# Performance work log

Hardware: AMD Instinct MI355X
Metric: run time of the kernel (lower is better)

Reference implementation:

```python
import jax, jax.numpy as jnp
import numpy as np

BN_EPS = 1e-5


def setup_inputs() -> dict:
    key = jax.random.key(0)
    k1, k2, k3, k4 = jax.random.split(key, 4)
    N, C, T, V = 32, 64, 300, 25
    K, O = 3, 64  # num_A adjacency branches, out_channels
    x = jax.random.normal(k1, (N, C, T, V), dtype=jnp.float32)
    A = jax.random.uniform(k2, (K, V, V), dtype=jnp.float32)
    # 1x1 conv weights per branch, He-style init as in conv_init (std = sqrt(2/O))
    W = jax.random.normal(k3, (K, O, C), dtype=jnp.float32) * np.sqrt(2.0 / O)
    b = jax.random.normal(k4, (K, O), dtype=jnp.float32) * 0.01
    gamma = jnp.ones((O,), dtype=jnp.float32)
    beta = jnp.zeros((O,), dtype=jnp.float32)
    return {"x": x, "A": A, "W": W, "b": b, "gamma": gamma, "beta": beta}


def reference(x, A, W, b, gamma, beta):
    # Per-branch graph aggregation over joints: xa[k] = x @ A[k] along V
    xa = jnp.einsum('nctv,kvw->knctw', x, A)            # [K,N,C,T,V]
    # Per-branch 1x1 conv (channel projection) + sum over branches
    y = jnp.einsum('koc,knctv->notv', W, xa)            # [N,O,T,V]
    y = y + b.sum(axis=0)[None, :, None, None]
    # BatchNorm2d in training mode: batch stats over (N,T,V), biased variance
    mean = jnp.mean(y, axis=(0, 2, 3), keepdims=True)
    var = jnp.mean((y - mean) ** 2, axis=(0, 2, 3), keepdims=True)
    y = (y - mean) * jax.lax.rsqrt(var + BN_EPS)
    y = y * gamma[None, :, None, None] + beta[None, :, None, None]
    return jax.nn.relu(y)
```

## Files before the change

kernel.cpp:

```cpp
#include <hip/hip_runtime.h>
#include <hip/hip_bf16.h>

#define NN 32
#define CC 64
#define TT 300
#define VV 25
#define KK 3
#define OO 64
#define TB 4
#define SB (TB * VV)
#define NREP 8

#define REP_OFF 0
#define WPK_OFF 1024
#define APK_OFF 7168
#define YBF_OFF 16384
#define YBF_BYTES ((size_t)NN * OO * TT * VV * 2)
#define WS_NEED_BF16 ((size_t)YBF_OFF * 4 + YBF_BYTES)

typedef __attribute__((ext_vector_type(8))) short short8;
typedef __attribute__((ext_vector_type(4))) float f32x4;

__device__ __forceinline__ unsigned short f2bf(float f) {
    unsigned u = __builtin_bit_cast(unsigned, f);
    u += 0x7FFFu + ((u >> 16) & 1u);
    return (unsigned short)(u >> 16);
}
__device__ __forceinline__ float bf2f(unsigned short b) {
    return __builtin_bit_cast(float, (unsigned)b << 16);
}
__device__ __forceinline__ unsigned pk2(float a, float b) {
    __hip_bfloat162 h = __float22bfloat162_rn(make_float2(a, b));
    unsigned r;
    __builtin_memcpy(&r, &h, sizeof(r));
    return r;
}

__global__ __launch_bounds__(512) void prep_pack(const float* __restrict__ A,
                                                 const float* __restrict__ W,
                                                 float* __restrict__ ws) {
    const int i = blockIdx.x * 512 + threadIdx.x;
    if (i < NREP * 128) ws[REP_OFF + i] = 0.0f;
    unsigned short* Wpk = reinterpret_cast<unsigned short*>(ws + WPK_OFF);
    unsigned short* Apk = reinterpret_cast<unsigned short*>(ws + APK_OFF);
    if (i < 1536) {
        int mt = i / 384, r = i - mt * 384;
        int kap = r / 64, lane = r - kap * 64;
        int li = lane & 15, g = lane >> 4;
        int o  = mt * 16 + li;
        int k  = kap >> 1, c0 = (kap & 1) * 32 + g * 8;
        const float* wp = W + ((size_t)(k * OO + o)) * CC + c0;
#pragma unroll
        for (int e = 0; e < 8; ++e) Wpk[i * 8 + e] = f2bf(wp[e]);
    } else if (i < 1920) {
        int j = i - 1536;
        int k = j / 128, r = j - k * 128;
        int nt = r / 64, lane = r - nt * 64;
        int li = lane & 15, g = lane >> 4;
        int w = nt * 16 + li;
#pragma unroll
        for (int e = 0; e < 8; ++e) {
            int v = g * 8 + e;
            float val = (v < VV && w < VV) ? A[(k * VV + v) * VV + w] : 0.0f;
            Apk[j * 8 + e] = f2bf(val);
        }
    }
}

template <int BF16Y>
__global__ __launch_bounds__(512, 6) void gcn_main(const float* __restrict__ x,
                                                   float* __restrict__ ws,
                                                   float* __restrict__ ypre) {
    __shared__ alignas(16) unsigned short xa_s[100 * 192];
    __shared__ float stats_s[128];

    const int bid  = blockIdx.x;
    const int n    = bid / (TT / TB);
    const int t0   = (bid % (TT / TB)) * TB;
    const int tid  = threadIdx.x;
    const int lane = tid & 63;
    const int wid  = tid >> 6;
    const int li   = lane & 15;
    const int g    = lane >> 4;

    if (tid < 128) stats_s[tid] = 0.0f;

    const float* xn = x + (size_t)n * (CC * TT * VV);
    short8 xf[2];
#pragma unroll
    for (int m = 0; m < 2; ++m) {
        const int row = (wid + 8 * m) * 16 + li;
        const int c = row & 63, t = row >> 6;
        const float* xr = xn + (size_t)c * (TT * VV) + (size_t)(t0 + t) * VV + g * 8;
        float e0, e1, e2, e3, e4, e5, e6, e7;
        if (g < 3) {
            e0 = xr[0]; e1 = xr[1]; e2 = xr[2]; e3 = xr[3];
            e4 = xr[4]; e5 = xr[5]; e6 = xr[6]; e7 = xr[7];
        } else {
            e0 = xr[0];
            e1 = e2 = e3 = e4 = e5 = e6 = e7 = 0.0f;
        }
        unsigned p[4] = {pk2(e0, e1), pk2(e2, e3), pk2(e4, e5), pk2(e6, e7)};
        __builtin_memcpy(&xf[m], p, 16);
    }

    short8 afrag[6];
#pragma unroll
    for (int kn = 0; kn < 6; ++kn)
        afrag[kn] = *reinterpret_cast<const short8*>(
            reinterpret_cast<const unsigned short*>(ws + APK_OFF) + ((size_t)kn * 64 + lane) * 8);

#pragma unroll
    for (int m = 0; m < 2; ++m) {
        const int mt = wid + 8 * m;
        const int r0 = mt * 16 + g * 4;
        const int tq = r0 >> 6, c0 = r0 & 63;
        const int sa = tq * 25 + li;
        const int w1 = 16 + li;
        const bool w1v = w1 < VV;
        const int sb = tq * 25 + w1;
        unsigned short* p0 = &xa_s[sa * 192 + (c0 ^ ((sa & 7) << 3))];
        unsigned short* p1 = &xa_s[(w1v ? sb : 0) * 192 + (c0 ^ (((w1v ? sb : 0) & 7) << 3))];
#pragma unroll
        for (int k = 0; k < KK; ++k) {
            f32x4 a0 = {0.f,0.f,0.f,0.f}, a1 = {0.f,0.f,0.f,0.f};
            a0 = __builtin_amdgcn_mfma_f32_16x16x32_bf16(xf[m], afrag[k * 2 + 0], a0, 0, 0, 0);
            a1 = __builtin_amdgcn_mfma_f32_16x16x32_bf16(xf[m], afrag[k * 2 + 1], a1, 0, 0, 0);
            uint2 q0 = make_uint2(pk2(a0[0], a0[1]), pk2(a0[2], a0[3]));
            *reinterpret_cast<uint2*>(p0 + k * 64) = q0;
            if (w1v) {
                uint2 q1 = make_uint2(pk2(a1[0], a1[1]), pk2(a1[2], a1[3]));
                *reinterpret_cast<uint2*>(p1 + k * 64) = q1;
            }
        }
    }
    __syncthreads();

    const int mtC   = wid >> 1;
    const int halfC = wid & 1;
    short8 wfr[6];
#pragma unroll
    for (int kap = 0; kap < 6; ++kap)
        wfr[kap] = *reinterpret_cast<const short8*>(
            reinterpret_cast<const unsigned short*>(ws + WPK_OFF) +
            ((size_t)(mtC * 6 + kap) * 64 + lane) * 8);

    unsigned short* ybf = reinterpret_cast<unsigned short*>(ws + YBF_OFF);
    const int ttv = TT * VV;
    const int oq  = mtC * 16 + g * 4;
    const int nNt = halfC ? 3 : 4;
    const int ntBase = halfC ? 4 : 0;
    float s1[4] = {0.f,0.f,0.f,0.f}, s2[4] = {0.f,0.f,0.f,0.f};
    for (int qq = 0; qq < nNt; ++qq) {
        const int nt = ntBase + qq;
        const int srow = nt * 16 + li;
        const bool sv = srow < SB;
        const int sr = sv ? srow : 0;
        const unsigned short* xb = &xa_s[sr * 192];
        const int sw = (sr & 7) << 3;
        f32x4 y = {0.f,0.f,0.f,0.f};
#pragma unroll
        for (int kap = 0; kap < 6; ++kap) {
            const short8 xaf = *reinterpret_cast<const short8*>(xb + ((kap * 32 + g * 8) ^ sw));
            y = __builtin_amdgcn_mfma_f32_16x16x32_bf16(wfr[kap], xaf, y, 0, 0, 0);
        }
        const size_t base = ((size_t)n * OO + oq) * ttv + (size_t)t0 * VV + srow;
        float vq[4];
        if (BF16Y) {
            unsigned p01 = pk2(y[0], y[1]);
            unsigned p23 = pk2(y[2], y[3]);
            if (sv) {
                ybf[base          ] = (unsigned short)p01;
                ybf[base +     ttv] = (unsigned short)(p01 >> 16);
                ybf[base + 2 * ttv] = (unsigned short)p23;
                ybf[base + 3 * ttv] = (unsigned short)(p23 >> 16);
            }
            vq[0] = bf2f((unsigned short)p01); vq[1] = bf2f((unsigned short)(p01 >> 16));
            vq[2] = bf2f((unsigned short)p23); vq[3] = bf2f((unsigned short)(p23 >> 16));
        } else {
            if (sv) {
                ypre[base          ] = y[0];
                ypre[base +     ttv] = y[1];
                ypre[base + 2 * ttv] = y[2];
                ypre[base + 3 * ttv] = y[3];
            }
            vq[0] = y[0]; vq[1] = y[1]; vq[2] = y[2]; vq[3] = y[3];
        }
#pragma unroll
        for (int j = 0; j < 4; ++j) {
            float v = sv ? vq[j] : 0.0f;
            s1[j] += v;
            s2[j] += v * v;
        }
    }
#pragma unroll
    for (int d = 1; d < 16; d <<= 1) {
#pragma unroll
        for (int j = 0; j < 4; ++j) {
            s1[j] += __shfl_xor(s1[j], d);
            s2[j] += __shfl_xor(s2[j], d);
        }
    }
    if (li == 0) {
#pragma unroll
        for (int j = 0; j < 4; ++j) {
            atomicAdd(&stats_s[oq + j], s1[j]);
            atomicAdd(&stats_s[64 + oq + j], s2[j]);
        }
    }
    __syncthreads();
    if (tid < 128)
        atomicAdd(&ws[REP_OFF + (bid & (NREP - 1)) * 128 + tid], stats_s[tid]);
}

template <int BF16Y>
__global__ __launch_bounds__(256) void bn_relu(float* __restrict__ out,
                                               const float* __restrict__ ws,
                                               const float* __restrict__ gamma,
                                               const float* __restrict__ beta) {
    const int i4 = blockIdx.x * 256 + threadIdx.x;
    const size_t i = (size_t)i4 * 4;
    const int o = (int)((i / (TT * VV)) % OO);

    float sum = 0.0f, sq = 0.0f;
#pragma unroll
    for (int r = 0; r < NREP; ++r) {
        sum += ws[REP_OFF + r * 128 + o];
        sq  += ws[REP_OFF + r * 128 + 64 + o];
    }
    const float cnt  = (float)NN * TT * VV;
    const float mean = sum / cnt;
    const float var  = sq / cnt - mean * mean;
    const float inv  = rsqrtf(var + 1e-5f);
    const float sc   = gamma[o] * inv;
    const float sh   = beta[o] - mean * sc;

    float4 v;
    if (BF16Y) {
        const ushort4 u = *reinterpret_cast<const ushort4*>(
            reinterpret_cast<const unsigned short*>(ws + YBF_OFF) + i);
        v.x = bf2f(u.x); v.y = bf2f(u.y); v.z = bf2f(u.z); v.w = bf2f(u.w);
    } else {
        v = *reinterpret_cast<float4*>(out + i);
    }
    v.x = fmaxf(v.x * sc + sh, 0.0f);
    v.y = fmaxf(v.y * sc + sh, 0.0f);
    v.z = fmaxf(v.z * sc + sh, 0.0f);
    v.w = fmaxf(v.w * sc + sh, 0.0f);
    *reinterpret_cast<float4*>(out + i) = v;
}

extern "C" void kernel_launch(void* const* d_in, const int* in_sizes, int n_in,
                              void* d_out, int out_size, void* d_ws, size_t ws_size,
                              hipStream_t stream) {
    const float* x     = (const float*)d_in[0];
    const float* A     = (const float*)d_in[1];
    const float* W     = (const float*)d_in[2];
    const float* gamma = (const float*)d_in[4];
    const float* beta  = (const float*)d_in[5];
    float* out = (float*)d_out;
    float* ws  = (float*)d_ws;

    const bool bf16y = ws_size >= WS_NEED_BF16;

    hipLaunchKernelGGL(prep_pack, dim3(4), dim3(512), 0, stream, A, W, ws);
    if (bf16y) {
        hipLaunchKernelGGL(HIP_KERNEL_NAME(gcn_main<1>), dim3(NN * (TT / TB)), dim3(512),
                           0, stream, x, ws, out);
        hipLaunchKernelGGL(HIP_KERNEL_NAME(bn_relu<1>), dim3((NN * OO * TT * VV) / 4 / 256),
                           dim3(256), 0, stream, out, ws, gamma, beta);
    } else {
        hipLaunchKernelGGL(HIP_KERNEL_NAME(gcn_main<0>), dim3(NN * (TT / TB)), dim3(512),
                           0, stream, x, ws, out);
        hipLaunchKernelGGL(HIP_KERNEL_NAME(bn_relu<0>), dim3((NN * OO * TT * VV) / 4 / 256),
                           dim3(256), 0, stream, out, ws, gamma, beta);
    }
}
```

Measured before the change: 57.40 us.

## Fuse GCN, BN stats and BN+ReLU into one cooperative persistent kernel

Adds a cooperative kernel with 480 persistent blocks that each process five (n,t) tiles. The pre-BN outputs stay in registers as packed bf16, and the batch statistics are reduced through a grid-wide sync before the normalize+ReLU is applied and written straight to the output. This removes the intermediate y round-trip through global memory and the separate bn_relu launch. In exchange it needs grid sync and enough occupancy for all 480 blocks (it falls back to the old path otherwise), the register pressure from holding five tiles of results is higher, and the output stores are scalar and strided.

```diff
diff --git a/kernel.cpp b/kernel.cpp
--- a/kernel.cpp
+++ b/kernel.cpp
@@ -1,5 +1,6 @@
 #include <hip/hip_runtime.h>
 #include <hip/hip_bf16.h>
+#include <hip/hip_cooperative_groups.h>
 
 #define NN 32
 #define CC 64
@@ -10,6 +11,9 @@
 #define TB 4
 #define SB (TB * VV)
 #define NREP 8
+#define NTILE (NN * (TT / TB))
+#define GRID 480
+#define TPB 5
 
 #define REP_OFF 0
 #define WPK_OFF 1024
@@ -67,6 +71,188 @@
     }
 }
 
+__global__ __launch_bounds__(512, 4) void gcn_coop(const float* __restrict__ x,
+                                                   float* __restrict__ ws,
+                                                   float* __restrict__ out,
+                                                   const float* __restrict__ gamma,
+                                                   const float* __restrict__ beta) {
+    __shared__ alignas(16) unsigned short xa_s[100 * 192];
+    __shared__ float stats_s[128];
+
+    const int bid  = blockIdx.x;
+    const int tid  = threadIdx.x;
+    const int lane = tid & 63;
+    const int wid  = tid >> 6;
+    const int li   = lane & 15;
+    const int g    = lane >> 4;
+    const int mtC   = wid >> 1;
+    const int halfC = wid & 1;
+    const int oq    = mtC * 16 + g * 4;
+    const int nNt   = halfC ? 3 : 4;
+    const int ntBase = halfC ? 4 : 0;
+    const int ttv = TT * VV;
+
+    if (tid < 128) stats_s[tid] = 0.0f;
+
+    short8 afrag[6], wfr[6];
+#pragma unroll
+    for (int kn = 0; kn < 6; ++kn)
+        afrag[kn] = *reinterpret_cast<const short8*>(
+            reinterpret_cast<const unsigned short*>(ws + APK_OFF) + ((size_t)kn * 64 + lane) * 8);
+#pragma unroll
+    for (int kap = 0; kap < 6; ++kap)
+        wfr[kap] = *reinterpret_cast<const short8*>(
+            reinterpret_cast<const unsigned short*>(ws + WPK_OFF) +
+            ((size_t)(mtC * 6 + kap) * 64 + lane) * 8);
+
+    unsigned yreg[TPB][4][2];
+    float s1[4] = {0.f,0.f,0.f,0.f}, s2[4] = {0.f,0.f,0.f,0.f};
+
+#pragma unroll
+    for (int ti = 0; ti < TPB; ++ti) {
+        const int tile = bid + ti * GRID;
+        const int n  = tile / (TT / TB);
+        const int t0 = (tile % (TT / TB)) * TB;
+        const float* xn = x + (size_t)n * (CC * ttv);
+
+        short8 xf[2];
+#pragma unroll
+        for (int m = 0; m < 2; ++m) {
+            const int row = (wid + 8 * m) * 16 + li;
+            const int c = row & 63, t = row >> 6;
+            const float* xr = xn + (size_t)c * ttv + (size_t)(t0 + t) * VV + g * 8;
+            float e0, e1, e2, e3, e4, e5, e6, e7;
+            if (g < 3) {
+                e0 = xr[0]; e1 = xr[1]; e2 = xr[2]; e3 = xr[3];
+                e4 = xr[4]; e5 = xr[5]; e6 = xr[6]; e7 = xr[7];
+            } else {
+                e0 = xr[0];
+                e1 = e2 = e3 = e4 = e5 = e6 = e7 = 0.0f;
+            }
+            unsigned p[4] = {pk2(e0, e1), pk2(e2, e3), pk2(e4, e5), pk2(e6, e7)};
+            __builtin_memcpy(&xf[m], p, 16);
+        }
+
+#pragma unroll
+        for (int m = 0; m < 2; ++m) {
+            const int mt = wid + 8 * m;
+            const int r0 = mt * 16 + g * 4;
+            const int tq = r0 >> 6, c0 = r0 & 63;
+            const int sa = tq * 25 + li;
+            const int w1 = 16 + li;
+            const bool w1v = w1 < VV;
+            const int sb = tq * 25 + w1;
+            unsigned short* p0 = &xa_s[sa * 192 + (c0 ^ ((sa & 7) << 3))];
+            unsigned short* p1 = &xa_s[(w1v ? sb : 0) * 192 + (c0 ^ (((w1v ? sb : 0) & 7) << 3))];
+#pragma unroll
+            for (int k = 0; k < KK; ++k) {
+                f32x4 a0 = {0.f,0.f,0.f,0.f}, a1 = {0.f,0.f,0.f,0.f};
+                a0 = __builtin_amdgcn_mfma_f32_16x16x32_bf16(xf[m], afrag[k * 2 + 0], a0, 0, 0, 0);
+                a1 = __builtin_amdgcn_mfma_f32_16x16x32_bf16(xf[m], afrag[k * 2 + 1], a1, 0, 0, 0);
+                uint2 q0 = make_uint2(pk2(a0[0], a0[1]), pk2(a0[2], a0[3]));
+                *reinterpret_cast<uint2*>(p0 + k * 64) = q0;
+                if (w1v) {
+                    uint2 q1 = make_uint2(pk2(a1[0], a1[1]), pk2(a1[2], a1[3]));
+                    *reinterpret_cast<uint2*>(p1 + k * 64) = q1;
+                }
+            }
+        }
+        __syncthreads();
+
+#pragma unroll
+        for (int qq = 0; qq < 4; ++qq) {
+            if (qq < nNt) {
+                const int nt = ntBase + qq;
+                const int srow = nt * 16 + li;
+                const bool sv = srow < SB;
+                const int sr = sv ? srow : 0;
+                const unsigned short* xb = &xa_s[sr * 192];
+                const int sw = (sr & 7) << 3;
+                f32x4 y = {0.f,0.f,0.f,0.f};
+#pragma unroll
+                for (int kap = 0; kap < 6; ++kap) {
+                    const short8 xaf = *reinterpret_cast<const short8*>(xb + ((kap * 32 + g * 8) ^ sw));
+                    y = __builtin_amdgcn_mfma_f32_16x16x32_bf16(wfr[kap], xaf, y, 0, 0, 0);
+                }
+                const unsigned p01 = pk2(y[0], y[1]);
+                const unsigned p23 = pk2(y[2], y[3]);
+                yreg[ti][qq][0] = p01;
+                yreg[ti][qq][1] = p23;
+                if (sv) {
+                    float v0 = bf2f((unsigned short)p01), v1 = bf2f((unsigned short)(p01 >> 16));
+                    float v2 = bf2f((unsigned short)p23), v3 = bf2f((unsigned short)(p23 >> 16));
+                    s1[0] += v0; s2[0] += v0 * v0;
+                    s1[1] += v1; s2[1] += v1 * v1;
+                    s1[2] += v2; s2[2] += v2 * v2;
+                    s1[3] += v3; s2[3] += v3 * v3;
+                }
+            }
+        }
+        __syncthreads();
+    }
+
+#pragma unroll
+    for (int d = 1; d < 16; d <<= 1) {
+#pragma unroll
+        for (int j = 0; j < 4; ++j) {
+            s1[j] += __shfl_xor(s1[j], d);
+            s2[j] += __shfl_xor(s2[j], d);
+        }
+    }
+    if (li == 0) {
+#pragma unroll
+        for (int j = 0; j < 4; ++j) {
+            atomicAdd(&stats_s[oq + j], s1[j]);
+            atomicAdd(&stats_s[64 + oq + j], s2[j]);
+        }
+    }
+    __syncthreads();
+    if (tid < 128)
+        atomicAdd(&ws[REP_OFF + (bid & (NREP - 1)) * 128 + tid], stats_s[tid]);
+
+    cooperative_groups::this_grid().sync();
+
+    if (tid < 128) {
+        float s = 0.0f;
+#pragma unroll
+        for (int r = 0; r < NREP; ++r) s += ws[REP_OFF + r * 128 + tid];
+        stats_s[tid] = s;
+    }
+    __syncthreads();
+    float sc[4], sh[4];
+    const float cnt = (float)NN * TT * VV;
+#pragma unroll
+    for (int j = 0; j < 4; ++j) {
+        const float mean = stats_s[oq + j] / cnt;
+        const float var  = stats_s[64 + oq + j] / cnt - mean * mean;
+        const float inv  = rsqrtf(var + 1e-5f);
+        sc[j] = gamma[oq + j] * inv;
+        sh[j] = beta[oq + j] - mean * sc[j];
+    }
+
+#pragma unroll
+    for (int ti = 0; ti < TPB; ++ti) {
+        const int tile = bid + ti * GRID;
+        const int n  = tile / (TT / TB);
+        const int t0 = (tile % (TT / TB)) * TB;
+#pragma unroll
+        for (int qq = 0; qq < 4; ++qq) {
+            if (qq < nNt) {
+                const int srow = (ntBase + qq) * 16 + li;
+                if (srow < SB) {
+                    const size_t base = ((size_t)n * OO + oq) * ttv + (size_t)t0 * VV + srow;
+                    const unsigned p01 = yreg[ti][qq][0];
+                    const unsigned p23 = yreg[ti][qq][1];
+                    out[base          ] = fmaxf(bf2f((unsigned short)p01) * sc[0] + sh[0], 0.0f);
+                    out[base +     ttv] = fmaxf(bf2f((unsigned short)(p01 >> 16)) * sc[1] + sh[1], 0.0f);
+                    out[base + 2 * ttv] = fmaxf(bf2f((unsigned short)p23) * sc[2] + sh[2], 0.0f);
+                    out[base + 3 * ttv] = fmaxf(bf2f((unsigned short)(p23 >> 16)) * sc[3] + sh[3], 0.0f);
+                }
+            }
+        }
+    }
+}
+
 template <int BF16Y>
 __global__ __launch_bounds__(512, 6) void gcn_main(const float* __restrict__ x,
                                                    float* __restrict__ ws,
@@ -261,18 +447,33 @@
     float* out = (float*)d_out;
     float* ws  = (float*)d_ws;
 
-    const bool bf16y = ws_size >= WS_NEED_BF16;
-
     hipLaunchKernelGGL(prep_pack, dim3(4), dim3(512), 0, stream, A, W, ws);
-    if (bf16y) {
-        hipLaunchKernelGGL(HIP_KERNEL_NAME(gcn_main<1>), dim3(NN * (TT / TB)), dim3(512),
-                           0, stream, x, ws, out);
-        hipLaunchKernelGGL(HIP_KERNEL_NAME(bn_relu<1>), dim3((NN * OO * TT * VV) / 4 / 256),
-                           dim3(256), 0, stream, out, ws, gamma, beta);
+
+    int maxB = 0;
+    hipError_t occErr = hipOccupancyMaxActiveBlocksPerMultiprocessor(
+        &maxB, reinterpret_cast<const void*>(&gcn_coop), 512, 0);
+    int dev = 0;
+    hipGetDevice(&dev);
+    int nCU = 0;
+    hipDeviceGetAttribute(&nCU, hipDeviceAttributeMultiprocessorCount, dev);
+    const bool coop_ok = (occErr == hipSuccess) && ((long)maxB * nCU >= GRID);
+
+    if (coop_ok) {
+        void* args[] = {(void*)&x, (void*)&ws, (void*)&out, (void*)&gamma, (void*)&beta};
+        hipLaunchCooperativeKernel(reinterpret_cast<const void*>(&gcn_coop),
+                                   dim3(GRID), dim3(512), args, 0, stream);
     } else {
-        hipLaunchKernelGGL(HIP_KERNEL_NAME(gcn_main<0>), dim3(NN * (TT / TB)), dim3(512),
-                           0, stream, x, ws, out);
-        hipLaunchKernelGGL(HIP_KERNEL_NAME(bn_relu<0>), dim3((NN * OO * TT * VV) / 4 / 256),
-                           dim3(256), 0, stream, out, ws, gamma, beta);
-    }
-}
+        const bool bf16y = ws_size >= WS_NEED_BF16;
+        if (bf16y) {
+            hipLaunchKernelGGL(HIP_KERNEL_NAME(gcn_main<1>), dim3(NTILE), dim3(512),
+                               0, stream, x, ws, out);
+            hipLaunchKernelGGL(HIP_KERNEL_NAME(bn_relu<1>), dim3((NN * OO * TT * VV) / 4 / 256),
+                               dim3(256), 0, stream, out, ws, gamma, beta);
+        } else {
+            hipLaunchKernelGGL(HIP_KERNEL_NAME(gcn_main<0>), dim3(NTILE), dim3(512),
+                               0, stream, x, ws, out);
+            hipLaunchKernelGGL(HIP_KERNEL_NAME(bn_relu<0>), dim3((NN * OO * TT * VV) / 4 / 256),
+                               dim3(256), 0, stream, out, ws, gamma, beta);
+        }
+    }
+}
```

Measured after the change: 57.43 us. About the same (+0.0%).

## Split main kernel into single-wave blocks, one time step each, with no barriers

Applied to the files above, without the earlier changes.

Restructures gcn_main from 512-thread blocks that each handle four time steps into 64-thread single-wavefront blocks that each handle one (n, t). The single wave does both the aggregation MFMAs and the projection MFMAs over all four output tiles, so the __syncthreads and the shared-memory stats reduction go away, and stats are added straight into global replica buffers (now 16 replicas). This cuts barrier overhead and LDS use per block, at the cost of four times as many blocks, more global atomics, and reloading the packed W fragments in every block.

```diff
diff --git a/kernel.cpp b/kernel.cpp
--- a/kernel.cpp
+++ b/kernel.cpp
@@ -7,13 +7,11 @@
 #define VV 25
 #define KK 3
 #define OO 64
-#define TB 4
-#define SB (TB * VV)
-#define NREP 8
+#define NREP 16
 
 #define REP_OFF 0
-#define WPK_OFF 1024
-#define APK_OFF 7168
+#define WPK_OFF 2048
+#define APK_OFF 8192
 #define YBF_OFF 16384
 #define YBF_BYTES ((size_t)NN * OO * TT * VV * 2)
 #define WS_NEED_BF16 ((size_t)YBF_OFF * 4 + YBF_BYTES)
@@ -68,30 +66,23 @@
 }
 
 template <int BF16Y>
-__global__ __launch_bounds__(512, 6) void gcn_main(const float* __restrict__ x,
-                                                   float* __restrict__ ws,
-                                                   float* __restrict__ ypre) {
-    __shared__ alignas(16) unsigned short xa_s[100 * 192];
-    __shared__ float stats_s[128];
+__global__ __launch_bounds__(64, 4) void gcn_main(const float* __restrict__ x,
+                                                  float* __restrict__ ws,
+                                                  float* __restrict__ ypre) {
+    __shared__ alignas(16) unsigned short xa_s[VV * 192];
 
     const int bid  = blockIdx.x;
-    const int n    = bid / (TT / TB);
-    const int t0   = (bid % (TT / TB)) * TB;
-    const int tid  = threadIdx.x;
-    const int lane = tid & 63;
-    const int wid  = tid >> 6;
+    const int n    = bid / TT;
+    const int t    = bid % TT;
+    const int lane = threadIdx.x;
     const int li   = lane & 15;
     const int g    = lane >> 4;
 
-    if (tid < 128) stats_s[tid] = 0.0f;
-
-    const float* xn = x + (size_t)n * (CC * TT * VV);
-    short8 xf[2];
-#pragma unroll
-    for (int m = 0; m < 2; ++m) {
-        const int row = (wid + 8 * m) * 16 + li;
-        const int c = row & 63, t = row >> 6;
-        const float* xr = xn + (size_t)c * (TT * VV) + (size_t)(t0 + t) * VV + g * 8;
+    short8 xf[4];
+#pragma unroll
+    for (int mt = 0; mt < 4; ++mt) {
+        const int c = mt * 16 + li;
+        const float* xr = x + (((size_t)n * CC + c) * TT + t) * VV + g * 8;
         float e0, e1, e2, e3, e4, e5, e6, e7;
         if (g < 3) {
             e0 = xr[0]; e1 = xr[1]; e2 = xr[2]; e3 = xr[3];
@@ -101,7 +92,7 @@
             e1 = e2 = e3 = e4 = e5 = e6 = e7 = 0.0f;
         }
         unsigned p[4] = {pk2(e0, e1), pk2(e2, e3), pk2(e4, e5), pk2(e6, e7)};
-        __builtin_memcpy(&xf[m], p, 16);
+        __builtin_memcpy(&xf[mt], p, 16);
     }
 
     short8 afrag[6];
@@ -111,21 +102,18 @@
             reinterpret_cast<const unsigned short*>(ws + APK_OFF) + ((size_t)kn * 64 + lane) * 8);
 
 #pragma unroll
-    for (int m = 0; m < 2; ++m) {
-        const int mt = wid + 8 * m;
-        const int r0 = mt * 16 + g * 4;
-        const int tq = r0 >> 6, c0 = r0 & 63;
-        const int sa = tq * 25 + li;
+    for (int mt = 0; mt < 4; ++mt) {
+        const int c0 = mt * 16 + g * 4;
+        const int sa = li;
         const int w1 = 16 + li;
         const bool w1v = w1 < VV;
-        const int sb = tq * 25 + w1;
         unsigned short* p0 = &xa_s[sa * 192 + (c0 ^ ((sa & 7) << 3))];
-        unsigned short* p1 = &xa_s[(w1v ? sb : 0) * 192 + (c0 ^ (((w1v ? sb : 0) & 7) << 3))];
+        unsigned short* p1 = &xa_s[(w1v ? w1 : 0) * 192 + (c0 ^ (((w1v ? w1 : 0) & 7) << 3))];
 #pragma unroll
         for (int k = 0; k < KK; ++k) {
             f32x4 a0 = {0.f,0.f,0.f,0.f}, a1 = {0.f,0.f,0.f,0.f};
-            a0 = __builtin_amdgcn_mfma_f32_16x16x32_bf16(xf[m], afrag[k * 2 + 0], a0, 0, 0, 0);
-            a1 = __builtin_amdgcn_mfma_f32_16x16x32_bf16(xf[m], afrag[k * 2 + 1], a1, 0, 0, 0);
+            a0 = __builtin_amdgcn_mfma_f32_16x16x32_bf16(xf[mt], afrag[k * 2 + 0], a0, 0, 0, 0);
+            a1 = __builtin_amdgcn_mfma_f32_16x16x32_bf16(xf[mt], afrag[k * 2 + 1], a1, 0, 0, 0);
             uint2 q0 = make_uint2(pk2(a0[0], a0[1]), pk2(a0[2], a0[3]));
             *reinterpret_cast<uint2*>(p0 + k * 64) = q0;
             if (w1v) {
@@ -134,83 +122,78 @@
             }
         }
     }
-    __syncthreads();
-
-    const int mtC   = wid >> 1;
-    const int halfC = wid & 1;
-    short8 wfr[6];
-#pragma unroll
-    for (int kap = 0; kap < 6; ++kap)
-        wfr[kap] = *reinterpret_cast<const short8*>(
-            reinterpret_cast<const unsigned short*>(ws + WPK_OFF) +
-            ((size_t)(mtC * 6 + kap) * 64 + lane) * 8);
 
     unsigned short* ybf = reinterpret_cast<unsigned short*>(ws + YBF_OFF);
     const int ttv = TT * VV;
-    const int oq  = mtC * 16 + g * 4;
-    const int nNt = halfC ? 3 : 4;
-    const int ntBase = halfC ? 4 : 0;
-    float s1[4] = {0.f,0.f,0.f,0.f}, s2[4] = {0.f,0.f,0.f,0.f};
-    for (int qq = 0; qq < nNt; ++qq) {
-        const int nt = ntBase + qq;
-        const int srow = nt * 16 + li;
-        const bool sv = srow < SB;
-        const int sr = sv ? srow : 0;
-        const unsigned short* xb = &xa_s[sr * 192];
-        const int sw = (sr & 7) << 3;
-        f32x4 y = {0.f,0.f,0.f,0.f};
-#pragma unroll
-        for (int kap = 0; kap < 6; ++kap) {
-            const short8 xaf = *reinterpret_cast<const short8*>(xb + ((kap * 32 + g * 8) ^ sw));
-            y = __builtin_amdgcn_mfma_f32_16x16x32_bf16(wfr[kap], xaf, y, 0, 0, 0);
-        }
-        const size_t base = ((size_t)n * OO + oq) * ttv + (size_t)t0 * VV + srow;
-        float vq[4];
-        if (BF16Y) {
-            unsigned p01 = pk2(y[0], y[1]);
-            unsigned p23 = pk2(y[2], y[3]);
-            if (sv) {
-                ybf[base          ] = (unsigned short)p01;
-                ybf[base +     ttv] = (unsigned short)(p01 >> 16);
-                ybf[base + 2 * ttv] = (unsigned short)p23;
-                ybf[base + 3 * ttv] = (unsigned short)(p23 >> 16);
-            }
-            vq[0] = bf2f((unsigned short)p01); vq[1] = bf2f((unsigned short)(p01 >> 16));
-            vq[2] = bf2f((unsigned short)p23); vq[3] = bf2f((unsigned short)(p23 >> 16));
-        } else {
-            if (sv) {
-                ypre[base          ] = y[0];
-                ypre[base +     ttv] = y[1];
-                ypre[base + 2 * ttv] = y[2];
-                ypre[base + 3 * ttv] = y[3];
-            }
-            vq[0] = y[0]; vq[1] = y[1]; vq[2] = y[2]; vq[3] = y[3];
-        }
-#pragma unroll
-        for (int j = 0; j < 4; ++j) {
-            float v = sv ? vq[j] : 0.0f;
-            s1[j] += v;
-            s2[j] += v * v;
-        }
-    }
-#pragma unroll
-    for (int d = 1; d < 16; d <<= 1) {
-#pragma unroll
-        for (int j = 0; j < 4; ++j) {
-            s1[j] += __shfl_xor(s1[j], d);
-            s2[j] += __shfl_xor(s2[j], d);
-        }
-    }
-    if (li == 0) {
-#pragma unroll
-        for (int j = 0; j < 4; ++j) {
-            atomicAdd(&stats_s[oq + j], s1[j]);
-            atomicAdd(&stats_s[64 + oq + j], s2[j]);
-        }
-    }
-    __syncthreads();
-    if (tid < 128)
-        atomicAdd(&ws[REP_OFF + (bid & (NREP - 1)) * 128 + tid], stats_s[tid]);
+    float* rep = ws + REP_OFF + (size_t)(bid & (NREP - 1)) * 128;
+#pragma unroll
+    for (int mt = 0; mt < 4; ++mt) {
+        short8 wfr[6];
+#pragma unroll
+        for (int kap = 0; kap < 6; ++kap)
+            wfr[kap] = *reinterpret_cast<const short8*>(
+                reinterpret_cast<const unsigned short*>(ws + WPK_OFF) +
+                ((size_t)(mt * 6 + kap) * 64 + lane) * 8);
+        const int oq = mt * 16 + g * 4;
+        float s1[4] = {0.f,0.f,0.f,0.f}, s2[4] = {0.f,0.f,0.f,0.f};
+#pragma unroll
+        for (int nt = 0; nt < 2; ++nt) {
+            const int srow = nt * 16 + li;
+            const bool sv = srow < VV;
+            const int sr = sv ? srow : 0;
+            const unsigned short* xb = &xa_s[sr * 192];
+            const int sw = (sr & 7) << 3;
+            f32x4 y = {0.f,0.f,0.f,0.f};
+#pragma unroll
+            for (int kap = 0; kap < 6; ++kap) {
+                const short8 xaf = *reinterpret_cast<const short8*>(xb + ((kap * 32 + g * 8) ^ sw));
+                y = __builtin_amdgcn_mfma_f32_16x16x32_bf16(wfr[kap], xaf, y, 0, 0, 0);
+            }
+            const size_t base = (((size_t)n * OO + oq) * TT + t) * VV + srow;
+            float vq[4];
+            if (BF16Y) {
+                unsigned p01 = pk2(y[0], y[1]);
+                unsigned p23 = pk2(y[2], y[3]);
+                if (sv) {
+                    ybf[base          ] = (unsigned short)p01;
+                    ybf[base +     ttv] = (unsigned short)(p01 >> 16);
+                    ybf[base + 2 * ttv] = (unsigned short)p23;
+                    ybf[base + 3 * ttv] = (unsigned short)(p23 >> 16);
+                }
+                vq[0] = bf2f((unsigned short)p01); vq[1] = bf2f((unsigned short)(p01 >> 16));
+                vq[2] = bf2f((unsigned short)p23); vq[3] = bf2f((unsigned short)(p23 >> 16));
+            } else {
+                if (sv) {
+                    ypre[base          ] = y[0];
+                    ypre[base +     ttv] = y[1];
+                    ypre[base + 2 * ttv] = y[2];
+                    ypre[base + 3 * ttv] = y[3];
+                }
+                vq[0] = y[0]; vq[1] = y[1]; vq[2] = y[2]; vq[3] = y[3];
+            }
+#pragma unroll
+            for (int j = 0; j < 4; ++j) {
+                float v = sv ? vq[j] : 0.0f;
+                s1[j] += v;
+                s2[j] += v * v;
+            }
+        }
+#pragma unroll
+        for (int d = 1; d < 16; d <<= 1) {
+#pragma unroll
+            for (int j = 0; j < 4; ++j) {
+                s1[j] += __shfl_xor(s1[j], d);
+                s2[j] += __shfl_xor(s2[j], d);
+            }
+        }
+        if (li == 0) {
+#pragma unroll
+            for (int j = 0; j < 4; ++j) {
+                atomicAdd(&rep[oq + j], s1[j]);
+                atomicAdd(&rep[64 + oq + j], s2[j]);
+            }
+        }
+    }
 }
 
 template <int BF16Y>
@@ -265,12 +248,12 @@
 
     hipLaunchKernelGGL(prep_pack, dim3(4), dim3(512), 0, stream, A, W, ws);
     if (bf16y) {
-        hipLaunchKernelGGL(HIP_KERNEL_NAME(gcn_main<1>), dim3(NN * (TT / TB)), dim3(512),
+        hipLaunchKernelGGL(HIP_KERNEL_NAME(gcn_main<1>), dim3(NN * TT), dim3(64),
                            0, stream, x, ws, out);
         hipLaunchKernelGGL(HIP_KERNEL_NAME(bn_relu<1>), dim3((NN * OO * TT * VV) / 4 / 256),
                            dim3(256), 0, stream, out, ws, gamma, beta);
     } else {
-        hipLaunchKernelGGL(HIP_KERNEL_NAME(gcn_main<0>), dim3(NN * (TT / TB)), dim3(512),
+        hipLaunchKernelGGL(HIP_KERNEL_NAME(gcn_main<0>), dim3(NN * TT), dim3(64),
                            0, stream, x, ws, out);
         hipLaunchKernelGGL(HIP_KERNEL_NAME(bn_relu<0>), dim3((NN * OO * TT * VV) / 4 / 256),
                            dim3(256), 0, stream, out, ws, gamma, beta);
```

Measured after the change: 111.5 us. +94.3%, slower.
